# Kernel optimization log

Hardware: AMD Instinct MI355X
Metric: run time of the kernel (lower is better)

## Reference

```python
import jax, jax.numpy as jnp
import numpy as np

B, SQ, SK, H, A = 4, 512, 512, 256, 128

def setup_inputs() -> dict:
    key = jax.random.key(0)
    ks = jax.random.split(key, 8)
    s = 1.0 / np.sqrt(H)
    sa = 1.0 / np.sqrt(A)
    return {
        "Q": jax.random.normal(ks[0], (B, SQ, H), dtype=jnp.float32),
        "K": jax.random.normal(ks[1], (B, SK, H), dtype=jnp.float32),
        "V": jax.random.normal(ks[2], (B, SK, H), dtype=jnp.float32),
        "W_q": jax.random.uniform(ks[3], (H, A), jnp.float32, -s, s),
        "W_k": jax.random.uniform(ks[4], (H, A), jnp.float32, -s, s),
        "v": jax.random.uniform(ks[5], (A,), jnp.float32, -sa, sa),
        "W_o": jax.random.uniform(ks[6], (H, H), jnp.float32, -s, s),
        "b_o": jax.random.uniform(ks[7], (H,), jnp.float32, -s, s),
    }

def reference(Q, K, V, W_q, W_k, v, W_o, b_o):
    # Q: (B, Sq, H), K/V: (B, Sk, H)
    Qt = Q @ W_q                      # (B, Sq, A)
    Kt = K @ W_k                      # (B, Sk, A)
    additive = jnp.tanh(Qt[:, :, None, :] + Kt[:, None, :, :])  # (B, Sq, Sk, A)
    scores = jnp.einsum('bqka,a->bqk', additive, v)             # (B, Sq, Sk)
    weights = jax.nn.softmax(scores, axis=-1)                   # (B, Sq, Sk)
    out = jnp.einsum('bqk,bkh->bqh', weights, V)                 # (B, Sq, H)
    out = out @ W_o + b_o
    return (out, weights)
```

## Files before the change

kernel.cpp:

```cpp
#include <hip/hip_runtime.h>
#include <math.h>

#define BB 4
#define SQL 512
#define SKL 512
#define HH 256
#define AA 128

#define PRESCALE 2.8853900817779268f
#define LOG2E    1.4426950408889634f

__device__ inline void fma4(float4& a, float s, const float4& b) {
    a.x = fmaf(s, b.x, a.x); a.y = fmaf(s, b.y, a.y);
    a.z = fmaf(s, b.z, a.z); a.w = fmaf(s, b.w, a.w);
}

template <int CTRL>
__device__ __forceinline__ float dpp_add(float x) {
    int m = __builtin_amdgcn_update_dpp(__float_as_int(x), __float_as_int(x),
                                        CTRL, 0xF, 0xF, false);
    return x + __int_as_float(m);
}
__device__ __forceinline__ float red8(float x) {
    x = dpp_add<0xB1>(x);
    x = dpp_add<0x4E>(x);
    x = dpp_add<0x141>(x);
    return x;
}

__global__ __launch_bounds__(256) void prep_kernel(
    const float* __restrict__ Q, const float* __restrict__ K,
    const float* __restrict__ V,
    const float* __restrict__ Wq, const float* __restrict__ Wk,
    const float* __restrict__ Wo,
    float* __restrict__ Qt, float* __restrict__ Kt, float* __restrict__ VW)
{
    __shared__ float rows[16 * HH];
    __shared__ float wl[64 * 128];
    int tid = threadIdx.x;
    int bid = blockIdx.x;

    const float* X; const float* W; float* Y;
    int ldW, ldY, col0, r0; float scale;
    if (bid < 128)      { X=Q; W=Wq; Y=Qt; ldW=AA; ldY=AA; col0=0; r0=bid*16;       scale=PRESCALE; }
    else if (bid < 256) { X=K; W=Wk; Y=Kt; ldW=AA; ldY=AA; col0=0; r0=(bid-128)*16; scale=PRESCALE; }
    else { int b2=bid-256; X=V; W=Wo; Y=VW; ldW=HH; ldY=HH; col0=(b2&1)*128; r0=(b2>>1)*16; scale=1.0f; }

    {
        const float4* Xv = (const float4*)(X + (size_t)r0 * HH);
        float4* rv = (float4*)rows;
        rv[tid]       = Xv[tid];
        rv[tid + 256] = Xv[tid + 256];
        rv[tid + 512] = Xv[tid + 512];
        rv[tid + 768] = Xv[tid + 768];
    }

    int r  = tid >> 5;
    int c4 = tid & 31;
    float4 accA = {0.f,0.f,0.f,0.f}, accB = {0.f,0.f,0.f,0.f};

    for (int ch = 0; ch < 4; ++ch) {
        __syncthreads();
        {
            const float* Wbase = W + (size_t)(ch * 64) * ldW + col0;
            float4* wv = (float4*)wl;
            #pragma unroll
            for (int it = 0; it < 8; ++it) {
                int l = tid + it * 256;
                wv[l] = *(const float4*)(Wbase + (size_t)(l >> 5) * ldW + ((l & 31) << 2));
            }
        }
        __syncthreads();
        const float* rrowA = rows + r * HH + ch * 64;
        const float* rrowB = rows + (r + 8) * HH + ch * 64;
        #pragma unroll 4
        for (int h4 = 0; h4 < 16; ++h4) {
            float4 ra = *(const float4*)(rrowA + h4 * 4);
            float4 rb = *(const float4*)(rrowB + h4 * 4);
            const float* wbase = wl + (h4 * 4) * 128 + (c4 << 2);
            float4 w0 = *(const float4*)(wbase);
            float4 w1 = *(const float4*)(wbase + 128);
            float4 w2 = *(const float4*)(wbase + 256);
            float4 w3 = *(const float4*)(wbase + 384);
            fma4(accA, ra.x, w0); fma4(accA, ra.y, w1);
            fma4(accA, ra.z, w2); fma4(accA, ra.w, w3);
            fma4(accB, rb.x, w0); fma4(accB, rb.y, w1);
            fma4(accB, rb.z, w2); fma4(accB, rb.w, w3);
        }
    }
    accA.x *= scale; accA.y *= scale; accA.z *= scale; accA.w *= scale;
    accB.x *= scale; accB.y *= scale; accB.z *= scale; accB.w *= scale;
    *(float4*)(Y + (size_t)(r0 + r)     * ldY + col0 + (c4 << 2)) = accA;
    *(float4*)(Y + (size_t)(r0 + r + 8) * ldY + col0 + (c4 << 2)) = accB;
}

__global__ __launch_bounds__(512, 2) void score_kernel(
    const float* __restrict__ Qt, const float* __restrict__ Kt,
    const float* __restrict__ v,  const float* __restrict__ VW,
    const float* __restrict__ bo,
    float* __restrict__ weights,  float* __restrict__ out)
{
    __shared__ float score[8][SKL];
    __shared__ float pout[8][4][HH];

    int tid = threadIdx.x;
    int b  = blockIdx.x >> 6;
    int q0 = (blockIdx.x & 63) << 3;
    int ag = tid & 7;
    int kl = tid >> 3;

    float Eq[8][16], v2[16];
    {
        const float4* vp = (const float4*)(v + ag * 16);
        #pragma unroll
        for (int j4 = 0; j4 < 4; ++j4) {
            float4 vv = vp[j4];
            v2[j4*4+0] = 2.0f*vv.x; v2[j4*4+1] = 2.0f*vv.y;
            v2[j4*4+2] = 2.0f*vv.z; v2[j4*4+3] = 2.0f*vv.w;
        }
        #pragma unroll
        for (int q = 0; q < 8; ++q) {
            const float4* qp = (const float4*)(Qt + (size_t)(b * SQL + q0 + q) * AA + ag * 16);
            #pragma unroll
            for (int j4 = 0; j4 < 4; ++j4) {
                float4 a = qp[j4];
                Eq[q][j4*4+0] = __builtin_amdgcn_exp2f(a.x);
                Eq[q][j4*4+1] = __builtin_amdgcn_exp2f(a.y);
                Eq[q][j4*4+2] = __builtin_amdgcn_exp2f(a.z);
                Eq[q][j4*4+3] = __builtin_amdgcn_exp2f(a.w);
            }
        }
    }

    float S_all;
    {
        float ls = 0.f;
        #pragma unroll
        for (int j = 0; j < 16; ++j) ls += v2[j];
        S_all = 0.5f * red8(ls);
    }

    const float* KtB = Kt + (size_t)b * SKL * AA;

    auto loadk = [&](float* kt, int c) {
        const float4* kt4 = (const float4*)(KtB + (size_t)(c * 64 + kl) * AA + ag * 16);
        *(float4*)&kt[0]  = kt4[0];
        *(float4*)&kt[4]  = kt4[1];
        *(float4*)&kt[8]  = kt4[2];
        *(float4*)&kt[12] = kt4[3];
    };

    auto compute = [&](const float* kt, int c) {
        float p[8];
        #pragma unroll
        for (int q = 0; q < 8; ++q) p[q] = 0.f;
        #pragma unroll
        for (int j = 0; j < 16; ++j) {
            float Ek = __builtin_amdgcn_exp2f(kt[j]);
            float vj = v2[j];
            #pragma unroll
            for (int q = 0; q < 8; ++q) {
                float r = __builtin_amdgcn_rcpf(fmaf(Ek, Eq[q][j], 1.0f));
                p[q] = fmaf(vj, r, p[q]);
            }
        }
        #pragma unroll
        for (int q = 0; q < 8; ++q) p[q] = red8(p[q]);
        if (ag == 0) {
            int k = c * 64 + kl;
            #pragma unroll
            for (int q = 0; q < 8; ++q)
                score[q][k] = (S_all - p[q]) * LOG2E;
        }
    };

    {
        float ktA[16], ktB_[16];
        loadk(ktA, 0);
        #pragma unroll 1
        for (int cc = 0; cc < 4; ++cc) {
            int c0 = cc * 2;
            loadk(ktB_, c0 + 1);
            compute(ktA, c0);
            if (cc != 3) loadk(ktA, c0 + 2);
            compute(ktB_, c0 + 1);
        }
    }
    __syncthreads();

    int wave = tid >> 6, lane = tid & 63;
    {
        int qi = wave;
        float ssum = 0.f;
        #pragma unroll
        for (int it = 0; it < 2; ++it) {
            int k0 = it * 256 + (lane << 2);
            float4 sv = *(float4*)&score[qi][k0];
            sv.x = __builtin_amdgcn_exp2f(sv.x);
            sv.y = __builtin_amdgcn_exp2f(sv.y);
            sv.z = __builtin_amdgcn_exp2f(sv.z);
            sv.w = __builtin_amdgcn_exp2f(sv.w);
            *(float4*)&score[qi][k0] = sv;
            ssum += (sv.x + sv.y) + (sv.z + sv.w);
        }
        #pragma unroll
        for (int off = 32; off; off >>= 1) ssum += __shfl_xor(ssum, off);
        float rinv = 1.0f / ssum;
        size_t rowoff = (size_t)(b * SQL + q0 + qi) * SKL;
        #pragma unroll
        for (int it = 0; it < 2; ++it) {
            int k0 = it * 256 + (lane << 2);
            float4 sv = *(float4*)&score[qi][k0];
            sv.x *= rinv; sv.y *= rinv; sv.z *= rinv; sv.w *= rinv;
            *(float4*)&score[qi][k0] = sv;
            *(float4*)(weights + rowoff + k0) = sv;
        }
    }
    __syncthreads();

    float4 acc[8];
    {
        #pragma unroll
        for (int q = 0; q < 8; ++q) acc[q] = make_float4(0.f, 0.f, 0.f, 0.f);
        const float4* VWb = (const float4*)(VW + (size_t)b * SKL * HH);
        int kbase = wave * 64;
        #pragma unroll 2
        for (int k4 = 0; k4 < 16; ++k4) {
            int kk = kbase + k4 * 4;
            float4 w[8];
            #pragma unroll
            for (int q = 0; q < 8; ++q) w[q] = *(const float4*)&score[q][kk];
            float4 vw;
            vw = VWb[(size_t)(kk + 0) * (HH/4) + lane];
            #pragma unroll
            for (int q = 0; q < 8; ++q) fma4(acc[q], w[q].x, vw);
            vw = VWb[(size_t)(kk + 1) * (HH/4) + lane];
            #pragma unroll
            for (int q = 0; q < 8; ++q) fma4(acc[q], w[q].y, vw);
            vw = VWb[(size_t)(kk + 2) * (HH/4) + lane];
            #pragma unroll
            for (int q = 0; q < 8; ++q) fma4(acc[q], w[q].z, vw);
            vw = VWb[(size_t)(kk + 3) * (HH/4) + lane];
            #pragma unroll
            for (int q = 0; q < 8; ++q) fma4(acc[q], w[q].w, vw);
        }
    }

    int h  = tid & 255;
    int qh = tid >> 8;
    float bias = bo[h];
    #pragma unroll
    for (int rnd = 0; rnd < 2; ++rnd) {
        #pragma unroll
        for (int q = 0; q < 4; ++q)
            *(float4*)&pout[wave][q][lane << 2] = acc[rnd * 4 + q];
        __syncthreads();
        #pragma unroll
        for (int qq = 0; qq < 2; ++qq) {
            int qi = qh * 2 + qq;
            float s = bias;
            #pragma unroll
            for (int w2 = 0; w2 < 8; ++w2) s += pout[w2][qi][h];
            out[(size_t)(b * SQL + q0 + rnd * 4 + qi) * HH + h] = s;
        }
        __syncthreads();
    }
}

extern "C" void kernel_launch(void* const* d_in, const int* in_sizes, int n_in,
                              void* d_out, int out_size, void* d_ws, size_t ws_size,
                              hipStream_t stream)
{
    const float* Q  = (const float*)d_in[0];
    const float* K  = (const float*)d_in[1];
    const float* V  = (const float*)d_in[2];
    const float* Wq = (const float*)d_in[3];
    const float* Wk = (const float*)d_in[4];
    const float* v  = (const float*)d_in[5];
    const float* Wo = (const float*)d_in[6];
    const float* bo = (const float*)d_in[7];

    float* out     = (float*)d_out;
    float* weights = out + (size_t)BB * SQL * HH;

    float* Qt = (float*)d_ws;
    float* Kt = Qt + (size_t)BB * SQL * AA;
    float* VW = Kt + (size_t)BB * SKL * AA;

    prep_kernel <<<512, 256, 0, stream>>>(Q, K, V, Wq, Wk, Wo, Qt, Kt, VW);
    score_kernel<<<256, 512, 0, stream>>>(Qt, Kt, v, VW, bo, weights, out);
}
```

Measured before the change: 114.3 us.

## Split the attention dimension across 16 lanes to shrink per-thread register state

The score phase now spreads the 128-wide attention dimension over 16 lanes of 8 elements each instead of 8 lanes of 16, so each thread holds half as many exp(Qt) values. The key loop runs 16 chunks of 32 keys with a simple one-ahead prefetch, and the reductions gain an extra DPP step (row_shr:8 style) to combine 16 lanes. Arrays are replaced with macro-expanded scalar and float4 variables to keep everything in registers and avoid scratch spills. The aim is to lower VGPR pressure under the 512x2 launch bound. The cost is one more cross-lane reduction step per score and more reduction work relative to the transcendental work.

```diff
diff --git a/kernel.cpp b/kernel.cpp
--- a/kernel.cpp
+++ b/kernel.cpp
@@ -21,10 +21,11 @@
                                         CTRL, 0xF, 0xF, false);
     return x + __int_as_float(m);
 }
-__device__ __forceinline__ float red8(float x) {
+__device__ __forceinline__ float red16(float x) {
     x = dpp_add<0xB1>(x);
     x = dpp_add<0x4E>(x);
     x = dpp_add<0x141>(x);
+    x = dpp_add<0x140>(x);
     return x;
 }
 
@@ -94,6 +95,8 @@
     *(float4*)(Y + (size_t)(r0 + r + 8) * ldY + col0 + (c4 << 2)) = accB;
 }
 
+#define FORQ(OP) OP(0) OP(1) OP(2) OP(3) OP(4) OP(5) OP(6) OP(7)
+
 __global__ __launch_bounds__(512, 2) void score_kernel(
     const float* __restrict__ Qt, const float* __restrict__ Kt,
     const float* __restrict__ v,  const float* __restrict__ VW,
@@ -106,84 +109,72 @@
     int tid = threadIdx.x;
     int b  = blockIdx.x >> 6;
     int q0 = (blockIdx.x & 63) << 3;
-    int ag = tid & 7;
-    int kl = tid >> 3;
-
-    float Eq[8][16], v2[16];
-    {
-        const float4* vp = (const float4*)(v + ag * 16);
-        #pragma unroll
-        for (int j4 = 0; j4 < 4; ++j4) {
-            float4 vv = vp[j4];
-            v2[j4*4+0] = 2.0f*vv.x; v2[j4*4+1] = 2.0f*vv.y;
-            v2[j4*4+2] = 2.0f*vv.z; v2[j4*4+3] = 2.0f*vv.w;
-        }
-        #pragma unroll
-        for (int q = 0; q < 8; ++q) {
-            const float4* qp = (const float4*)(Qt + (size_t)(b * SQL + q0 + q) * AA + ag * 16);
-            #pragma unroll
-            for (int j4 = 0; j4 < 4; ++j4) {
-                float4 a = qp[j4];
-                Eq[q][j4*4+0] = __builtin_amdgcn_exp2f(a.x);
-                Eq[q][j4*4+1] = __builtin_amdgcn_exp2f(a.y);
-                Eq[q][j4*4+2] = __builtin_amdgcn_exp2f(a.z);
-                Eq[q][j4*4+3] = __builtin_amdgcn_exp2f(a.w);
+    int ag = tid & 15;
+    int kl = tid >> 4;
+
+    float4 v2a, v2b;
+    {
+        const float4* vp = (const float4*)(v + ag * 8);
+        v2a = vp[0]; v2b = vp[1];
+        v2a.x *= 2.f; v2a.y *= 2.f; v2a.z *= 2.f; v2a.w *= 2.f;
+        v2b.x *= 2.f; v2b.y *= 2.f; v2b.z *= 2.f; v2b.w *= 2.f;
+    }
+
+#define DECL_EQ(Qi) float4 EqA##Qi, EqB##Qi;
+    FORQ(DECL_EQ)
+#define LOAD_EQ(Qi) { \
+        const float4* qp = (const float4*)(Qt + (size_t)(b * SQL + q0 + Qi) * AA + ag * 8); \
+        float4 t0 = qp[0], t1 = qp[1]; \
+        (EqA##Qi).x = __builtin_amdgcn_exp2f(t0.x); (EqA##Qi).y = __builtin_amdgcn_exp2f(t0.y); \
+        (EqA##Qi).z = __builtin_amdgcn_exp2f(t0.z); (EqA##Qi).w = __builtin_amdgcn_exp2f(t0.w); \
+        (EqB##Qi).x = __builtin_amdgcn_exp2f(t1.x); (EqB##Qi).y = __builtin_amdgcn_exp2f(t1.y); \
+        (EqB##Qi).z = __builtin_amdgcn_exp2f(t1.z); (EqB##Qi).w = __builtin_amdgcn_exp2f(t1.w); }
+    FORQ(LOAD_EQ)
+
+    float S_all;
+    {
+        float ls = (v2a.x + v2a.y) + (v2a.z + v2a.w)
+                 + (v2b.x + v2b.y) + (v2b.z + v2b.w);
+        S_all = 0.5f * red16(ls);
+    }
+
+    const float4* ktp = (const float4*)(Kt + (size_t)b * SKL * AA);
+
+    {
+        float4 ka = ktp[(size_t)kl * (AA / 4) + ag * 2];
+        float4 kb = ktp[(size_t)kl * (AA / 4) + ag * 2 + 1];
+        #pragma unroll 1
+        for (int c = 0; c < 16; ++c) {
+            float4 na, nb;
+            if (c < 15) {
+                int kn = (c + 1) * 32 + kl;
+                na = ktp[(size_t)kn * (AA / 4) + ag * 2];
+                nb = ktp[(size_t)kn * (AA / 4) + ag * 2 + 1];
             }
-        }
-    }
-
-    float S_all;
-    {
-        float ls = 0.f;
-        #pragma unroll
-        for (int j = 0; j < 16; ++j) ls += v2[j];
-        S_all = 0.5f * red8(ls);
-    }
-
-    const float* KtB = Kt + (size_t)b * SKL * AA;
-
-    auto loadk = [&](float* kt, int c) {
-        const float4* kt4 = (const float4*)(KtB + (size_t)(c * 64 + kl) * AA + ag * 16);
-        *(float4*)&kt[0]  = kt4[0];
-        *(float4*)&kt[4]  = kt4[1];
-        *(float4*)&kt[8]  = kt4[2];
-        *(float4*)&kt[12] = kt4[3];
-    };
-
-    auto compute = [&](const float* kt, int c) {
-        float p[8];
-        #pragma unroll
-        for (int q = 0; q < 8; ++q) p[q] = 0.f;
-        #pragma unroll
-        for (int j = 0; j < 16; ++j) {
-            float Ek = __builtin_amdgcn_exp2f(kt[j]);
-            float vj = v2[j];
-            #pragma unroll
-            for (int q = 0; q < 8; ++q) {
-                float r = __builtin_amdgcn_rcpf(fmaf(Ek, Eq[q][j], 1.0f));
-                p[q] = fmaf(vj, r, p[q]);
+#define DECL_P(Qi) float p##Qi = 0.f;
+            FORQ(DECL_P)
+#define STEP(KE, VE, HB, COMP) { \
+            float Ek = __builtin_amdgcn_exp2f(KE); \
+            p0 = fmaf(VE, __builtin_amdgcn_rcpf(fmaf(Ek, (Eq##HB##0).COMP, 1.0f)), p0); \
+            p1 = fmaf(VE, __builtin_amdgcn_rcpf(fmaf(Ek, (Eq##HB##1).COMP, 1.0f)), p1); \
+            p2 = fmaf(VE, __builtin_amdgcn_rcpf(fmaf(Ek, (Eq##HB##2).COMP, 1.0f)), p2); \
+            p3 = fmaf(VE, __builtin_amdgcn_rcpf(fmaf(Ek, (Eq##HB##3).COMP, 1.0f)), p3); \
+            p4 = fmaf(VE, __builtin_amdgcn_rcpf(fmaf(Ek, (Eq##HB##4).COMP, 1.0f)), p4); \
+            p5 = fmaf(VE, __builtin_amdgcn_rcpf(fmaf(Ek, (Eq##HB##5).COMP, 1.0f)), p5); \
+            p6 = fmaf(VE, __builtin_amdgcn_rcpf(fmaf(Ek, (Eq##HB##6).COMP, 1.0f)), p6); \
+            p7 = fmaf(VE, __builtin_amdgcn_rcpf(fmaf(Ek, (Eq##HB##7).COMP, 1.0f)), p7); }
+            STEP(ka.x, v2a.x, A, x) STEP(ka.y, v2a.y, A, y)
+            STEP(ka.z, v2a.z, A, z) STEP(ka.w, v2a.w, A, w)
+            STEP(kb.x, v2b.x, B, x) STEP(kb.y, v2b.y, B, y)
+            STEP(kb.z, v2b.z, B, z) STEP(kb.w, v2b.w, B, w)
+#define RED_P(Qi) p##Qi = red16(p##Qi);
+            FORQ(RED_P)
+            if (ag == 0) {
+                int k = c * 32 + kl;
+#define STORE_P(Qi) score[Qi][k] = (S_all - p##Qi) * LOG2E;
+                FORQ(STORE_P)
             }
-        }
-        #pragma unroll
-        for (int q = 0; q < 8; ++q) p[q] = red8(p[q]);
-        if (ag == 0) {
-            int k = c * 64 + kl;
-            #pragma unroll
-            for (int q = 0; q < 8; ++q)
-                score[q][k] = (S_all - p[q]) * LOG2E;
-        }
-    };
-
-    {
-        float ktA[16], ktB_[16];
-        loadk(ktA, 0);
-        #pragma unroll 1
-        for (int cc = 0; cc < 4; ++cc) {
-            int c0 = cc * 2;
-            loadk(ktB_, c0 + 1);
-            compute(ktA, c0);
-            if (cc != 3) loadk(ktA, c0 + 2);
-            compute(ktB_, c0 + 1);
+            ka = na; kb = nb;
         }
     }
     __syncthreads();
@@ -218,52 +209,63 @@
     }
     __syncthreads();
 
-    float4 acc[8];
-    {
-        #pragma unroll
-        for (int q = 0; q < 8; ++q) acc[q] = make_float4(0.f, 0.f, 0.f, 0.f);
+#define DECL_ACC(Qi) float4 acc##Qi = {0.f, 0.f, 0.f, 0.f};
+    FORQ(DECL_ACC)
+    {
         const float4* VWb = (const float4*)(VW + (size_t)b * SKL * HH);
         int kbase = wave * 64;
         #pragma unroll 2
         for (int k4 = 0; k4 < 16; ++k4) {
             int kk = kbase + k4 * 4;
-            float4 w[8];
-            #pragma unroll
-            for (int q = 0; q < 8; ++q) w[q] = *(const float4*)&score[q][kk];
+#define DECL_W(Qi) float4 w##Qi = *(const float4*)&score[Qi][kk];
+            FORQ(DECL_W)
             float4 vw;
-            vw = VWb[(size_t)(kk + 0) * (HH/4) + lane];
-            #pragma unroll
-            for (int q = 0; q < 8; ++q) fma4(acc[q], w[q].x, vw);
-            vw = VWb[(size_t)(kk + 1) * (HH/4) + lane];
-            #pragma unroll
-            for (int q = 0; q < 8; ++q) fma4(acc[q], w[q].y, vw);
-            vw = VWb[(size_t)(kk + 2) * (HH/4) + lane];
-            #pragma unroll
-            for (int q = 0; q < 8; ++q) fma4(acc[q], w[q].z, vw);
-            vw = VWb[(size_t)(kk + 3) * (HH/4) + lane];
-            #pragma unroll
-            for (int q = 0; q < 8; ++q) fma4(acc[q], w[q].w, vw);
+            vw = VWb[(size_t)(kk + 0) * (HH / 4) + lane];
+#define FMA_X(Qi) fma4(acc##Qi, (w##Qi).x, vw);
+            FORQ(FMA_X)
+            vw = VWb[(size_t)(kk + 1) * (HH / 4) + lane];
+#define FMA_Y(Qi) fma4(acc##Qi, (w##Qi).y, vw);
+            FORQ(FMA_Y)
+            vw = VWb[(size_t)(kk + 2) * (HH / 4) + lane];
+#define FMA_Z(Qi) fma4(acc##Qi, (w##Qi).z, vw);
+            FORQ(FMA_Z)
+            vw = VWb[(size_t)(kk + 3) * (HH / 4) + lane];
+#define FMA_W(Qi) fma4(acc##Qi, (w##Qi).w, vw);
+            FORQ(FMA_W)
         }
     }
 
     int h  = tid & 255;
     int qh = tid >> 8;
     float bias = bo[h];
+
+    *(float4*)&pout[wave][0][lane << 2] = acc0;
+    *(float4*)&pout[wave][1][lane << 2] = acc1;
+    *(float4*)&pout[wave][2][lane << 2] = acc2;
+    *(float4*)&pout[wave][3][lane << 2] = acc3;
+    __syncthreads();
     #pragma unroll
-    for (int rnd = 0; rnd < 2; ++rnd) {
-        #pragma unroll
-        for (int q = 0; q < 4; ++q)
-            *(float4*)&pout[wave][q][lane << 2] = acc[rnd * 4 + q];
-        __syncthreads();
-        #pragma unroll
-        for (int qq = 0; qq < 2; ++qq) {
-            int qi = qh * 2 + qq;
-            float s = bias;
-            #pragma unroll
-            for (int w2 = 0; w2 < 8; ++w2) s += pout[w2][qi][h];
-            out[(size_t)(b * SQL + q0 + rnd * 4 + qi) * HH + h] = s;
-        }
-        __syncthreads();
+    for (int qq = 0; qq < 2; ++qq) {
+        int qi = qh * 2 + qq;
+        float s = bias;
+        #pragma unroll
+        for (int w2 = 0; w2 < 8; ++w2) s += pout[w2][qi][h];
+        out[(size_t)(b * SQL + q0 + qi) * HH + h] = s;
+    }
+    __syncthreads();
+
+    *(float4*)&pout[wave][0][lane << 2] = acc4;
+    *(float4*)&pout[wave][1][lane << 2] = acc5;
+    *(float4*)&pout[wave][2][lane << 2] = acc6;
+    *(float4*)&pout[wave][3][lane << 2] = acc7;
+    __syncthreads();
+    #pragma unroll
+    for (int qq = 0; qq < 2; ++qq) {
+        int qi = qh * 2 + qq;
+        float s = bias;
+        #pragma unroll
+        for (int w2 = 0; w2 < 8; ++w2) s += pout[w2][qi][h];
+        out[(size_t)(b * SQL + q0 + 4 + qi) * HH + h] = s;
     }
 }
 
```

New measurement: 119.8 us. +4.8%, slower.
